# Kernel tuning notes

Hardware: AMD Instinct MI355X
Metric: run time of the kernel (lower is better)

The kernel has to match this reference:

```python
import jax, jax.numpy as jnp
import numpy as np

NEG_SLOPE = 0.2


def gat_layer(x, W, att_src, att_dst, bias, src, dst, N):
    # x: [N, Din], W: [Din, H*C], att_src/att_dst: [H, C], bias: [H*C]
    H, C = att_src.shape
    h = (x @ W).reshape(N, H, C)                       # [N, H, C]
    a_s = jnp.einsum('nhc,hc->nh', h, att_src)          # [N, H]
    a_d = jnp.einsum('nhc,hc->nh', h, att_dst)          # [N, H]
    e = jax.nn.leaky_relu(a_s[src] + a_d[dst], NEG_SLOPE)  # [E, H]
    # segment softmax over incoming edges of each destination node
    m = jax.ops.segment_max(e, dst, num_segments=N)     # [N, H]
    p = jnp.exp(e - m[dst])                             # [E, H]
    denom = jax.ops.segment_sum(p, dst, num_segments=N)  # [N, H]
    alpha = p / denom[dst]                              # [E, H]
    msg = alpha[:, :, None] * h[src]                    # [E, H, C]
    out = jax.ops.segment_sum(msg, dst, num_segments=N)  # [N, H, C]
    return out.reshape(N, H * C) + bias


def setup_inputs() -> dict:
    key = jax.random.key(0)
    N, E, D, H, C = 50000, 1600000, 128, 4, 32
    ks = jax.random.split(key, 12)
    x = jax.random.normal(ks[0], (N, D), dtype=jnp.float32)
    edge_index = jax.random.randint(ks[1], (2, E), 0, N, dtype=jnp.int64)
    s1 = 1.0 / np.sqrt(D)
    W1 = jax.random.normal(ks[2], (D, H * C), dtype=jnp.float32) * s1
    att_src1 = jax.random.normal(ks[3], (H, C), dtype=jnp.float32) * (1.0 / np.sqrt(C))
    att_dst1 = jax.random.normal(ks[4], (H, C), dtype=jnp.float32) * (1.0 / np.sqrt(C))
    bias1 = jnp.zeros((H * C,), dtype=jnp.float32)
    s2 = 1.0 / np.sqrt(H * C)
    W2 = jax.random.normal(ks[5], (H * C, 1), dtype=jnp.float32) * s2
    att_src2 = jax.random.normal(ks[6], (1, 1), dtype=jnp.float32)
    att_dst2 = jax.random.normal(ks[7], (1, 1), dtype=jnp.float32)
    bias2 = jnp.zeros((1,), dtype=jnp.float32)
    return {
        'x': x, 'edge_index': edge_index,
        'W1': W1, 'att_src1': att_src1, 'att_dst1': att_dst1, 'bias1': bias1,
        'W2': W2, 'att_src2': att_src2, 'att_dst2': att_dst2, 'bias2': bias2,
    }


def reference(x, edge_index, W1, att_src1, att_dst1, bias1, W2, att_src2, att_dst2, bias2):
    N = x.shape[0]
    # PyG GATConv default: add self-loops
    loop = jnp.arange(N, dtype=edge_index.dtype)
    src = jnp.concatenate([edge_index[0], loop])
    dst = jnp.concatenate([edge_index[1], loop])
    # dropout(p=0.5) is identity in eval mode
    h = gat_layer(x, W1, att_src1, att_dst1, bias1, src, dst, N)   # [N, H*C]
    h = jax.nn.elu(h)
    out = gat_layer(h, W2, att_src2, att_dst2, bias2, src, dst, N)  # [N, 1]
    return out.squeeze(-1)  # [N]
```

## Files before the change

kernel.cpp:

```cpp
#include <hip/hip_runtime.h>
#include <hip/hip_fp16.h>
#include <stdint.h>

#define NEG_SLOPE 0.2f
#define BSHIFT 7
#define NB 256

__device__ __forceinline__ float lrelu(float x){ return x > 0.f ? x : NEG_SLOPE * x; }
__device__ __forceinline__ float elu1(float x){ return x > 0.f ? x : expm1f(x); }
__device__ __forceinline__ unsigned fenc(float f){
  unsigned u = __float_as_uint(f);
  return (u & 0x80000000u) ? ~u : (u | 0x80000000u);
}
__device__ __forceinline__ float fdec(unsigned u){
  return (u & 0x80000000u) ? __uint_as_float(u & 0x7fffffffu) : __uint_as_float(~u);
}

__global__ __launch_bounds__(256) void k_gemm1_hist(
    const float* __restrict__ x, const float* __restrict__ W1,
    const float* __restrict__ atts, const float* __restrict__ attd,
    __half* __restrict__ h1, float* __restrict__ as1, float* __restrict__ ad1,
    float* __restrict__ gblkmax,
    const int* __restrict__ ei, int* __restrict__ gcnt,
    int E, int N, int B, int chunk, int G){
  __shared__ float xs[128 * 128];
  if (blockIdx.x >= G){
    int bid = blockIdx.x - G;
    int* hist = (int*)xs;
    for (int t = threadIdx.x; t < B; t += 256) hist[t] = 0;
    __syncthreads();
    int T = E + N;
    int lo = bid * chunk;
    int hi = min(lo + chunk, T);
    for (int i = lo + (int)threadIdx.x; i < hi; i += 256){
      int d = (i < E) ? ei[E + i] : (i - E);
      atomicAdd(&hist[d >> BSHIFT], 1);
    }
    __syncthreads();
    for (int t = threadIdx.x; t < B; t += 256) gcnt[bid * B + t] = hist[t];
    return;
  }
  int n0 = blockIdx.x * 128;
  int t = threadIdx.x;
  {
    int row = t & 127;
    int kc = t >> 7;
    int n = n0 + row;
    const float4* x4 = (const float4*)x;
    #pragma unroll 4
    for (int i = 0; i < 16; ++i){
      float4 v = (n < N) ? x4[(size_t)n * 32 + kc * 16 + i]
                         : make_float4(0.f, 0.f, 0.f, 0.f);
      int k = kc * 64 + 4 * i;
      xs[(k + 0) * 128 + row] = v.x;
      xs[(k + 1) * 128 + row] = v.y;
      xs[(k + 2) * 128 + row] = v.z;
      xs[(k + 3) * 128 + row] = v.w;
    }
  }
  __syncthreads();
  int m = t & 15;
  int rg = t >> 4;
  int rb = rg * 8;
  const float4* W14 = (const float4*)W1;
  float acc[8][8];
  #pragma unroll
  for (int r = 0; r < 8; ++r)
    #pragma unroll
    for (int c = 0; c < 8; ++c) acc[r][c] = 0.f;
  #pragma unroll 2
  for (int k = 0; k < 128; ++k){
    float4 w0 = W14[k * 32 + 2 * m];
    float4 w1 = W14[k * 32 + 2 * m + 1];
    float4 xa = *(const float4*)&xs[k * 128 + rb];
    float4 xb = *(const float4*)&xs[k * 128 + rb + 4];
    float xr[8] = {xa.x, xa.y, xa.z, xa.w, xb.x, xb.y, xb.z, xb.w};
    float wc[8] = {w0.x, w0.y, w0.z, w0.w, w1.x, w1.y, w1.z, w1.w};
    #pragma unroll
    for (int r = 0; r < 8; ++r)
      #pragma unroll
      for (int c = 0; c < 8; ++c)
        acc[r][c] = fmaf(xr[r], wc[c], acc[r][c]);
  }
  float4 av0 = ((const float4*)atts)[2 * m], av1 = ((const float4*)atts)[2 * m + 1];
  float4 dv0 = ((const float4*)attd)[2 * m], dv1 = ((const float4*)attd)[2 * m + 1];
  int h = m >> 2;
  float lmax = -INFINITY;
  #pragma unroll
  for (int r = 0; r < 8; ++r){
    int n = n0 + rb + r;
    if (n < N){
      union { __half2 hh[4]; float4 f; } u;
      u.hh[0] = __floats2half2_rn(acc[r][0], acc[r][1]);
      u.hh[1] = __floats2half2_rn(acc[r][2], acc[r][3]);
      u.hh[2] = __floats2half2_rn(acc[r][4], acc[r][5]);
      u.hh[3] = __floats2half2_rn(acc[r][6], acc[r][7]);
      *(float4*)(h1 + (size_t)n * 128 + 8 * m) = u.f;
    }
    float s  = acc[r][0]*av0.x + acc[r][1]*av0.y + acc[r][2]*av0.z + acc[r][3]*av0.w
             + acc[r][4]*av1.x + acc[r][5]*av1.y + acc[r][6]*av1.z + acc[r][7]*av1.w;
    float dd = acc[r][0]*dv0.x + acc[r][1]*dv0.y + acc[r][2]*dv0.z + acc[r][3]*dv0.w
             + acc[r][4]*dv1.x + acc[r][5]*dv1.y + acc[r][6]*dv1.z + acc[r][7]*dv1.w;
    s  += __shfl_down(s, 1);  s  += __shfl_down(s, 2);
    dd += __shfl_down(dd, 1); dd += __shfl_down(dd, 2);
    lmax = fmaxf(lmax, s);
    if ((m & 3) == 0 && n < N){
      as1[n * 4 + h] = s;
      ad1[n * 4 + h] = dd;
    }
  }
  __syncthreads();
  if ((m & 3) == 0) xs[(m >> 2) * 16 + rg] = lmax;
  __syncthreads();
  if (t < 4){
    float mx = xs[t * 16];
    #pragma unroll
    for (int i = 1; i < 16; ++i) mx = fmaxf(mx, xs[t * 16 + i]);
    gblkmax[blockIdx.x * 4 + t] = mx;
  }
}

__global__ void k_bprefix(const int* __restrict__ gcnt, int* __restrict__ ecur,
                          int* __restrict__ btot, int B){
  int b = blockIdx.x;
  int t = threadIdx.x;
  int v = gcnt[t * B + b];
  int lane = t & 63, wid = t >> 6;
  int x = v;
  #pragma unroll
  for (int off = 1; off < 64; off <<= 1){
    int tmp = __shfl_up(x, off, 64);
    if (lane >= off) x += tmp;
  }
  __shared__ int ws[4];
  if (lane == 63) ws[wid] = x;
  __syncthreads();
  if (t == 0){
    int s = 0;
    #pragma unroll
    for (int i = 0; i < 4; ++i){ int tmp = ws[i]; ws[i] = s; s += tmp; }
  }
  __syncthreads();
  int excl = ws[wid] + x - v;
  ecur[b * NB + t] = excl;
  if (t == 255) btot[b] = excl + v;
}

__global__ void k_btscan(const int* __restrict__ btot, int* __restrict__ bstart,
                         const float* __restrict__ gblkmax, float* __restrict__ asmaxf,
                         unsigned* __restrict__ h2mm, int B, int T){
  __shared__ int wsum[16];
  __shared__ int carry_s;
  __shared__ unsigned smenc[4];
  int lane = threadIdx.x & 63, wid = threadIdx.x >> 6;
  if (threadIdx.x == 0) carry_s = 0;
  if (threadIdx.x < 4) smenc[threadIdx.x] = 0u;
  __syncthreads();
  for (int base = 0; base < B; base += 1024){
    int i = base + (int)threadIdx.x;
    int v = (i < B) ? btot[i] : 0;
    int x = v;
    #pragma unroll
    for (int off = 1; off < 64; off <<= 1){
      int t = __shfl_up(x, off, 64);
      if (lane >= off) x += t;
    }
    if (lane == 63) wsum[wid] = x;
    __syncthreads();
    if (wid == 0 && lane < 16){
      int w = wsum[lane];
      #pragma unroll
      for (int off = 1; off < 16; off <<= 1){
        int t = __shfl_up(w, off, 64);
        if (lane >= off) w += t;
      }
      wsum[lane] = w;
    }
    __syncthreads();
    int carry = carry_s;
    int prefix = carry + (wid ? wsum[wid - 1] : 0);
    if (i < B) bstart[i] = prefix + x - v;
    __syncthreads();
    if (threadIdx.x == 1023) carry_s = carry + wsum[15];
    __syncthreads();
  }
  if (threadIdx.x == 0) bstart[B] = T;
  float lmax = -INFINITY;
  for (int i = threadIdx.x; i < B * 4; i += 1024) lmax = fmaxf(lmax, gblkmax[i]);
  atomicMax(&smenc[threadIdx.x & 3], fenc(lmax));
  __syncthreads();
  if (threadIdx.x < 4) asmaxf[threadIdx.x] = fdec(smenc[threadIdx.x]);
  if (threadIdx.x < 2) h2mm[threadIdx.x] = 0u;
}

__global__ void k_bscatter(const int* __restrict__ ei, const int* __restrict__ ecur,
                           const int* __restrict__ bstart,
                           unsigned* __restrict__ ebuf,
                           int E, int N, int B, int chunk){
  __shared__ int cur[512];
  for (int t = threadIdx.x; t < B; t += 256)
    cur[t] = ecur[t * NB + blockIdx.x] + bstart[t];
  __syncthreads();
  int T = E + N;
  int lo = blockIdx.x * chunk;
  int hi = min(lo + chunk, T);
  for (int i = lo + (int)threadIdx.x; i < hi; i += 256){
    int s, d;
    if (i < E){ s = ei[i]; d = ei[E + i]; } else { s = d = i - E; }
    int pos = atomicAdd(&cur[d >> BSHIFT], 1);
    ebuf[pos] = ((unsigned)(d & 127) << 25) | (unsigned)s;
  }
}

__global__ void k_bfinal(const unsigned* __restrict__ ebuf,
                         const int* __restrict__ bstart,
                         int* __restrict__ csr, int* __restrict__ rs,
                         int N, int B, int T){
  int b = blockIdx.x;
  int d0 = b << BSHIFT;
  int dcount = min(128, N - d0);
  int ebeg = bstart[b];
  int eend = bstart[b + 1];
  __shared__ int hist[128];
  __shared__ int excl[128];
  if (threadIdx.x < 128) hist[threadIdx.x] = 0;
  __syncthreads();
  for (int i = ebeg + (int)threadIdx.x; i < eend; i += 256)
    atomicAdd(&hist[ebuf[i] >> 25], 1);
  __syncthreads();
  if (threadIdx.x < 64){
    int l = threadIdx.x;
    int v0 = hist[l], v1 = hist[l + 64];
    int s0 = v0, s1 = v1;
    #pragma unroll
    for (int off = 1; off < 64; off <<= 1){
      int t0 = __shfl_up(s0, off, 64); if (l >= off) s0 += t0;
      int t1 = __shfl_up(s1, off, 64); if (l >= off) s1 += t1;
    }
    int tot0 = __shfl(s0, 63, 64);
    excl[l] = s0 - v0;
    excl[l + 64] = tot0 + s1 - v1;
  }
  __syncthreads();
  if (threadIdx.x < dcount) rs[d0 + threadIdx.x] = ebeg + excl[threadIdx.x];
  if (threadIdx.x < 128) hist[threadIdx.x] = excl[threadIdx.x];
  if (b == 0 && threadIdx.x == 255) rs[N] = T;
  __syncthreads();
  for (int i = ebeg + (int)threadIdx.x; i < eend; i += 256){
    unsigned e = ebuf[i];
    int pos = ebeg + atomicAdd(&hist[e >> 25], 1);
    csr[pos] = (int)(e & 0x01FFFFFFu);
  }
}

__global__ void k_agg1(const int* __restrict__ csr, const int* __restrict__ rs,
                       const float* __restrict__ as1, const float* __restrict__ ad1,
                       const float* __restrict__ asmaxf,
                       const float4* __restrict__ h1,
                       const float* __restrict__ bias1,
                       const float* __restrict__ W2, float* __restrict__ h2, int N){
  int wv = threadIdx.x >> 6;
  int lane = threadIdx.x & 63;
  int d = blockIdx.x * 4 + wv;
  if (d >= N) return;
  int g = lane >> 4;
  int m = lane & 15;
  int h = m >> 2;
  float adh = ad1[d * 4 + h];
  float M = lrelu(asmaxf[h] + adh);
  int beg = rs[d], end = rs[d + 1];
  float den = 0.f;
  float a0=0.f,a1=0.f,a2=0.f,a3=0.f,a4=0.f,a5=0.f,a6=0.f,a7=0.f;
  int j = beg;
  for (; j + 8 <= end; j += 8){
    int sA = csr[j + g];
    int sB = csr[j + 4 + g];
    float eA = lrelu(as1[sA * 4 + h] + adh);
    float eB = lrelu(as1[sB * 4 + h] + adh);
    float pA = __expf(eA - M);
    float pB = __expf(eB - M);
    float4 rA = h1[(size_t)sA * 16 + m];
    float4 rB = h1[(size_t)sB * 16 + m];
    den += pA + pB;
    float2 cA0 = __half22float2(*(__half2*)&rA.x);
    float2 cA1 = __half22float2(*(__half2*)&rA.y);
    float2 cA2 = __half22float2(*(__half2*)&rA.z);
    float2 cA3 = __half22float2(*(__half2*)&rA.w);
    a0 = fmaf(pA, cA0.x, a0); a1 = fmaf(pA, cA0.y, a1);
    a2 = fmaf(pA, cA1.x, a2); a3 = fmaf(pA, cA1.y, a3);
    a4 = fmaf(pA, cA2.x, a4); a5 = fmaf(pA, cA2.y, a5);
    a6 = fmaf(pA, cA3.x, a6); a7 = fmaf(pA, cA3.y, a7);
    float2 cB0 = __half22float2(*(__half2*)&rB.x);
    float2 cB1 = __half22float2(*(__half2*)&rB.y);
    float2 cB2 = __half22float2(*(__half2*)&rB.z);
    float2 cB3 = __half22float2(*(__half2*)&rB.w);
    a0 = fmaf(pB, cB0.x, a0); a1 = fmaf(pB, cB0.y, a1);
    a2 = fmaf(pB, cB1.x, a2); a3 = fmaf(pB, cB1.y, a3);
    a4 = fmaf(pB, cB2.x, a4); a5 = fmaf(pB, cB2.y, a5);
    a6 = fmaf(pB, cB3.x, a6); a7 = fmaf(pB, cB3.y, a7);
  }
  for (; j < end; j += 4){
    int slot = j + g;
    bool v = slot < end;
    int s = csr[v ? slot : beg];
    float e = lrelu(as1[s * 4 + h] + adh);
    float p = v ? __expf(e - M) : 0.f;
    float4 raw = h1[(size_t)s * 16 + m];
    float2 c0 = __half22float2(*(__half2*)&raw.x);
    float2 c1 = __half22float2(*(__half2*)&raw.y);
    float2 c2 = __half22float2(*(__half2*)&raw.z);
    float2 c3 = __half22float2(*(__half2*)&raw.w);
    den += p;
    a0 = fmaf(p, c0.x, a0); a1 = fmaf(p, c0.y, a1);
    a2 = fmaf(p, c1.x, a2); a3 = fmaf(p, c1.y, a3);
    a4 = fmaf(p, c2.x, a4); a5 = fmaf(p, c2.y, a5);
    a6 = fmaf(p, c3.x, a6); a7 = fmaf(p, c3.y, a7);
  }
  #define CMB(v) v += __shfl_xor(v, 16); v += __shfl_xor(v, 32);
  CMB(a0) CMB(a1) CMB(a2) CMB(a3) CMB(a4) CMB(a5) CMB(a6) CMB(a7) CMB(den)
  #undef CMB
  float part = 0.f;
  if (lane < 16){
    float invden = 1.f / den;
    float4 b03 = ((const float4*)bias1)[2 * m];
    float4 b47 = ((const float4*)bias1)[2 * m + 1];
    float4 w03 = ((const float4*)W2)[2 * m];
    float4 w47 = ((const float4*)W2)[2 * m + 1];
    part  = elu1(a0 * invden + b03.x) * w03.x;
    part += elu1(a1 * invden + b03.y) * w03.y;
    part += elu1(a2 * invden + b03.z) * w03.z;
    part += elu1(a3 * invden + b03.w) * w03.w;
    part += elu1(a4 * invden + b47.x) * w47.x;
    part += elu1(a5 * invden + b47.y) * w47.y;
    part += elu1(a6 * invden + b47.z) * w47.z;
    part += elu1(a7 * invden + b47.w) * w47.w;
  }
  #pragma unroll
  for (int off = 8; off; off >>= 1) part += __shfl_down(part, off);
  if (lane == 0) h2[d] = part;
}

__global__ void k_h2mm(const float* __restrict__ h2, unsigned* __restrict__ h2mm, int N){
  float mx = -INFINITY, mn = INFINITY;
  for (int i = blockIdx.x * blockDim.x + threadIdx.x; i < N; i += gridDim.x * blockDim.x){
    float v = h2[i];
    mx = fmaxf(mx, v); mn = fminf(mn, v);
  }
  #pragma unroll
  for (int off = 1; off < 64; off <<= 1){
    mx = fmaxf(mx, __shfl_xor(mx, off));
    mn = fminf(mn, __shfl_xor(mn, off));
  }
  if ((threadIdx.x & 63) == 0){
    atomicMax(&h2mm[0], fenc(mx));
    atomicMax(&h2mm[1], fenc(-mn));
  }
}

__global__ void k_agg2(const int* __restrict__ csr, const int* __restrict__ rs,
                       const float* __restrict__ h2, const unsigned* __restrict__ h2mm,
                       const float* __restrict__ as2p, const float* __restrict__ ad2p,
                       const float* __restrict__ bias2, float* __restrict__ out, int N){
  int grp = threadIdx.x >> 4;
  int l16 = threadIdx.x & 15;
  int d = blockIdx.x * 16 + grp;
  if (d >= N) return;
  float asc = as2p[0];
  float hmax = fdec(h2mm[0]), hmn = -fdec(h2mm[1]);
  float bound = (asc >= 0.f) ? asc * hmax : asc * hmn;
  float hd = h2[d] * ad2p[0];
  float M = lrelu(bound + hd);
  int beg = rs[d], end = rs[d + 1];
  float den = 0.f, acc = 0.f;
  for (int j = beg + l16; j < end; j += 16){
    float hs = h2[csr[j]];
    float p = __expf(lrelu(hs * asc + hd) - M);
    den += p;
    acc = fmaf(p, hs, acc);
  }
  #pragma unroll
  for (int off = 8; off; off >>= 1){
    den += __shfl_xor(den, off, 16);
    acc += __shfl_xor(acc, off, 16);
  }
  if (l16 == 0) out[d] = acc / den + bias2[0];
}

extern "C" void kernel_launch(void* const* d_in, const int* in_sizes, int n_in,
                              void* d_out, int out_size, void* d_ws, size_t ws_size,
                              hipStream_t stream){
  const float* x     = (const float*)d_in[0];
  const int*   ei    = (const int*)  d_in[1];
  const float* W1    = (const float*)d_in[2];
  const float* atts1 = (const float*)d_in[3];
  const float* attd1 = (const float*)d_in[4];
  const float* bias1 = (const float*)d_in[5];
  const float* W2    = (const float*)d_in[6];
  const float* atts2 = (const float*)d_in[7];
  const float* attd2 = (const float*)d_in[8];
  const float* bias2 = (const float*)d_in[9];

  int N = in_sizes[0] / 128;
  int E = in_sizes[1] / 2;
  int T = E + N;
  int B = (N + 127) >> BSHIFT;
  int chunk = (T + NB - 1) / NB;
  int G = (N + 127) / 128;

  uintptr_t base = (uintptr_t)d_ws;
  auto take = [&](size_t bytes) -> uintptr_t {
    base = (base + 255) & ~(uintptr_t)255;
    uintptr_t r = base;
    base += bytes;
    return r;
  };
  __half* h1     = (__half*)  take((size_t)N * 128 * 2);
  unsigned* ebuf = (unsigned*)take((size_t)T * 4);
  float*  as1    = (float*)   take((size_t)N * 4 * 4);
  float*  ad1    = (float*)   take((size_t)N * 4 * 4);
  float*  h2     = (float*)   take((size_t)N * 4);
  int*    gcnt   = (int*)     take((size_t)NB * B * 4);
  int*    ecur   = (int*)     take((size_t)NB * B * 4);
  int*    csr    = (int*)     take((size_t)T * 4);
  int*    rs     = (int*)     take((size_t)(N + 1) * 4);
  int*    btot   = (int*)     take((size_t)B * 4);
  int*    bstart = (int*)     take((size_t)(B + 1) * 4);
  float*  gblkmax= (float*)   take((size_t)G * 4 * 4);
  float*  asmaxf = (float*)   take(4 * 4);
  unsigned* h2mm = (unsigned*)take(2 * 4);

  k_gemm1_hist<<<G + NB, 256, 0, stream>>>(x, W1, atts1, attd1, h1, as1, ad1,
                                           gblkmax, ei, gcnt, E, N, B, chunk, G);
  k_bprefix <<<B, 256, 0, stream>>>(gcnt, ecur, btot, B);
  k_btscan  <<<1, 1024, 0, stream>>>(btot, bstart, gblkmax, asmaxf, h2mm, B, T);
  k_bscatter<<<NB, 256, 0, stream>>>(ei, ecur, bstart, ebuf, E, N, B, chunk);
  k_bfinal  <<<B, 256, 0, stream>>>(ebuf, bstart, csr, rs, N, B, T);
  k_agg1    <<<(N + 3) / 4, 256, 0, stream>>>(csr, rs, as1, ad1, asmaxf,
                                              (const float4*)h1, bias1, W2, h2, N);
  k_h2mm    <<<64, 256, 0, stream>>>(h2, h2mm, N);
  k_agg2    <<<(N + 15) / 16, 256, 0, stream>>>(csr, rs, h2, h2mm, atts2, attd2,
                                                bias2, (float*)d_out, N);
}
```

Before: 163.0 us.

## Remove single-block bucket-total scan kernel by recomputing scan per block

Drops the serial single-block k_btscan launch: each k_bscatter and k_bfinal block now recomputes the exclusive scan of bucket totals (B<=512) in shared memory, and the global max reduction moves into block 0 of k_bprefix. It also raises the scatter and finalize kernels to 512 threads per block. This removes one launch and a serialized dependency step, at the cost of redundant per-block scan work and the assumption that B fits in 512.

```diff
diff --git a/kernel.cpp b/kernel.cpp
--- a/kernel.cpp
+++ b/kernel.cpp
@@ -121,7 +121,12 @@
 }
 
 __global__ void k_bprefix(const int* __restrict__ gcnt, int* __restrict__ ecur,
-                          int* __restrict__ btot, int B){
+                          int* __restrict__ btot,
+                          const float* __restrict__ gblkmax,
+                          float* __restrict__ asmaxf, unsigned* __restrict__ h2mm,
+                          int B, int G4){
+  __shared__ int ws[4];
+  __shared__ unsigned smenc[4];
   int b = blockIdx.x;
   int t = threadIdx.x;
   int v = gcnt[t * B + b];
@@ -132,8 +137,8 @@
     int tmp = __shfl_up(x, off, 64);
     if (lane >= off) x += tmp;
   }
-  __shared__ int ws[4];
   if (lane == 63) ws[wid] = x;
+  if (t < 4) smenc[t] = 0u;
   __syncthreads();
   if (t == 0){
     int s = 0;
@@ -144,67 +149,54 @@
   int excl = ws[wid] + x - v;
   ecur[b * NB + t] = excl;
   if (t == 255) btot[b] = excl + v;
-}
-
-__global__ void k_btscan(const int* __restrict__ btot, int* __restrict__ bstart,
-                         const float* __restrict__ gblkmax, float* __restrict__ asmaxf,
-                         unsigned* __restrict__ h2mm, int B, int T){
-  __shared__ int wsum[16];
-  __shared__ int carry_s;
-  __shared__ unsigned smenc[4];
-  int lane = threadIdx.x & 63, wid = threadIdx.x >> 6;
-  if (threadIdx.x == 0) carry_s = 0;
-  if (threadIdx.x < 4) smenc[threadIdx.x] = 0u;
-  __syncthreads();
-  for (int base = 0; base < B; base += 1024){
-    int i = base + (int)threadIdx.x;
-    int v = (i < B) ? btot[i] : 0;
-    int x = v;
-    #pragma unroll
-    for (int off = 1; off < 64; off <<= 1){
-      int t = __shfl_up(x, off, 64);
-      if (lane >= off) x += t;
-    }
-    if (lane == 63) wsum[wid] = x;
+  if (b == 0){
+    float lmax = -INFINITY;
+    for (int i = t; i < G4; i += 256) lmax = fmaxf(lmax, gblkmax[i]);
+    atomicMax(&smenc[t & 3], fenc(lmax));
     __syncthreads();
-    if (wid == 0 && lane < 16){
-      int w = wsum[lane];
-      #pragma unroll
-      for (int off = 1; off < 16; off <<= 1){
-        int t = __shfl_up(w, off, 64);
-        if (lane >= off) w += t;
-      }
-      wsum[lane] = w;
-    }
-    __syncthreads();
-    int carry = carry_s;
-    int prefix = carry + (wid ? wsum[wid - 1] : 0);
-    if (i < B) bstart[i] = prefix + x - v;
-    __syncthreads();
-    if (threadIdx.x == 1023) carry_s = carry + wsum[15];
-    __syncthreads();
-  }
-  if (threadIdx.x == 0) bstart[B] = T;
-  float lmax = -INFINITY;
-  for (int i = threadIdx.x; i < B * 4; i += 1024) lmax = fmaxf(lmax, gblkmax[i]);
-  atomicMax(&smenc[threadIdx.x & 3], fenc(lmax));
-  __syncthreads();
-  if (threadIdx.x < 4) asmaxf[threadIdx.x] = fdec(smenc[threadIdx.x]);
-  if (threadIdx.x < 2) h2mm[threadIdx.x] = 0u;
-}
-
-__global__ void k_bscatter(const int* __restrict__ ei, const int* __restrict__ ecur,
-                           const int* __restrict__ bstart,
-                           unsigned* __restrict__ ebuf,
-                           int E, int N, int B, int chunk){
+    if (t < 4) asmaxf[t] = fdec(smenc[t]);
+    if (t < 2) h2mm[t] = 0u;
+  }
+}
+
+__device__ __forceinline__ void local_btot_scan(const int* __restrict__ btot,
+                                                int* sc, int* wsum8, int B){
+  int tid = threadIdx.x;
+  int lane = tid & 63, wid = tid >> 6;
+  int v = (tid < B) ? btot[tid] : 0;
+  int x = v;
+  #pragma unroll
+  for (int off = 1; off < 64; off <<= 1){
+    int tmp = __shfl_up(x, off, 64);
+    if (lane >= off) x += tmp;
+  }
+  if (lane == 63) wsum8[wid] = x;
+  __syncthreads();
+  if (tid == 0){
+    int s = 0;
+    #pragma unroll
+    for (int i = 0; i < 8; ++i){ int tmp = wsum8[i]; wsum8[i] = s; s += tmp; }
+  }
+  __syncthreads();
+  sc[tid] = wsum8[wid] + x - v;
+  __syncthreads();
+}
+
+__global__ __launch_bounds__(512) void k_bscatter(
+    const int* __restrict__ ei, const int* __restrict__ ecur,
+    const int* __restrict__ btot, unsigned* __restrict__ ebuf,
+    int E, int N, int B, int chunk){
+  __shared__ int sc[512];
+  __shared__ int wsum8[8];
   __shared__ int cur[512];
-  for (int t = threadIdx.x; t < B; t += 256)
-    cur[t] = ecur[t * NB + blockIdx.x] + bstart[t];
+  local_btot_scan(btot, sc, wsum8, B);
+  int tid = threadIdx.x;
+  if (tid < B) cur[tid] = ecur[tid * NB + blockIdx.x] + sc[tid];
   __syncthreads();
   int T = E + N;
   int lo = blockIdx.x * chunk;
   int hi = min(lo + chunk, T);
-  for (int i = lo + (int)threadIdx.x; i < hi; i += 256){
+  for (int i = lo + tid; i < hi; i += 512){
     int s, d;
     if (i < E){ s = ei[i]; d = ei[E + i]; } else { s = d = i - E; }
     int pos = atomicAdd(&cur[d >> BSHIFT], 1);
@@ -212,20 +204,23 @@
   }
 }
 
-__global__ void k_bfinal(const unsigned* __restrict__ ebuf,
-                         const int* __restrict__ bstart,
-                         int* __restrict__ csr, int* __restrict__ rs,
-                         int N, int B, int T){
+__global__ __launch_bounds__(512) void k_bfinal(
+    const unsigned* __restrict__ ebuf, const int* __restrict__ btot,
+    int* __restrict__ csr, int* __restrict__ rs,
+    int N, int B, int T){
+  __shared__ int sc[512];
+  __shared__ int wsum8[8];
+  __shared__ int hist[128];
+  __shared__ int excl[128];
+  local_btot_scan(btot, sc, wsum8, B);
   int b = blockIdx.x;
   int d0 = b << BSHIFT;
   int dcount = min(128, N - d0);
-  int ebeg = bstart[b];
-  int eend = bstart[b + 1];
-  __shared__ int hist[128];
-  __shared__ int excl[128];
+  int ebeg = sc[b];
+  int eend = (b + 1 < B) ? sc[b + 1] : T;
   if (threadIdx.x < 128) hist[threadIdx.x] = 0;
   __syncthreads();
-  for (int i = ebeg + (int)threadIdx.x; i < eend; i += 256)
+  for (int i = ebeg + (int)threadIdx.x; i < eend; i += 512)
     atomicAdd(&hist[ebuf[i] >> 25], 1);
   __syncthreads();
   if (threadIdx.x < 64){
@@ -246,7 +241,7 @@
   if (threadIdx.x < 128) hist[threadIdx.x] = excl[threadIdx.x];
   if (b == 0 && threadIdx.x == 255) rs[N] = T;
   __syncthreads();
-  for (int i = ebeg + (int)threadIdx.x; i < eend; i += 256){
+  for (int i = ebeg + (int)threadIdx.x; i < eend; i += 512){
     unsigned e = ebuf[i];
     int pos = ebeg + atomicAdd(&hist[e >> 25], 1);
     csr[pos] = (int)(e & 0x01FFFFFFu);
@@ -424,17 +419,15 @@
   int*    csr    = (int*)     take((size_t)T * 4);
   int*    rs     = (int*)     take((size_t)(N + 1) * 4);
   int*    btot   = (int*)     take((size_t)B * 4);
-  int*    bstart = (int*)     take((size_t)(B + 1) * 4);
   float*  gblkmax= (float*)   take((size_t)G * 4 * 4);
   float*  asmaxf = (float*)   take(4 * 4);
   unsigned* h2mm = (unsigned*)take(2 * 4);
 
   k_gemm1_hist<<<G + NB, 256, 0, stream>>>(x, W1, atts1, attd1, h1, as1, ad1,
                                            gblkmax, ei, gcnt, E, N, B, chunk, G);
-  k_bprefix <<<B, 256, 0, stream>>>(gcnt, ecur, btot, B);
-  k_btscan  <<<1, 1024, 0, stream>>>(btot, bstart, gblkmax, asmaxf, h2mm, B, T);
-  k_bscatter<<<NB, 256, 0, stream>>>(ei, ecur, bstart, ebuf, E, N, B, chunk);
-  k_bfinal  <<<B, 256, 0, stream>>>(ebuf, bstart, csr, rs, N, B, T);
+  k_bprefix <<<B, 256, 0, stream>>>(gcnt, ecur, btot, gblkmax, asmaxf, h2mm, B, G * 4);
+  k_bscatter<<<NB, 512, 0, stream>>>(ei, ecur, btot, ebuf, E, N, B, chunk);
+  k_bfinal  <<<B, 512, 0, stream>>>(ebuf, btot, csr, rs, N, B, T);
   k_agg1    <<<(N + 3) / 4, 256, 0, stream>>>(csr, rs, as1, ad1, asmaxf,
                                               (const float4*)h1, bias1, W2, h2, N);
   k_h2mm    <<<64, 256, 0, stream>>>(h2, h2mm, N);
```

Result: faster. 148.1 us (-9.1%).
